# Optimization experiments

Measured on AMD Instinct MI355X. Metric: run time of the kernel, lower is better.

## Reference

```python
import jax, jax.numpy as jnp
import numpy as np

B, N, F_IN, D, DEPTH = 16, 1024, 80, 64, 4
BN_EPS = 1e-5

def setup_inputs() -> dict:
    key = jax.random.key(0)
    ks = jax.random.split(key, 24)
    def xavier(k, shape, gain):
        fan_in, fan_out = shape[0], shape[-1]
        a = gain * np.sqrt(6.0 / (fan_in + fan_out))
        return jax.random.uniform(k, shape, jnp.float32, -a, a)
    g_relu = float(np.sqrt(2.0))
    g_lrelu = float(np.sqrt(2.0 / (1 + 0.01 ** 2)))
    adj = jax.random.randint(ks[0], (B, N, N), 0, 2, jnp.int32)
    X = jax.random.normal(ks[1], (B, N, F_IN), jnp.float32)
    root_list = jax.random.randint(ks[2], (B, DEPTH, N), 0, 2).astype(jnp.float32)
    W0 = xavier(ks[3], (F_IN, D), g_lrelu)
    Wl = jnp.stack([xavier(ks[4 + i], (D, D), g_relu) for i in range(3)])
    a1l = jnp.stack([xavier(ks[7 + i], (D, 1), g_relu)[:, 0] for i in range(3)])
    a2l = jnp.stack([xavier(ks[10 + i], (D, 1), g_relu)[:, 0] for i in range(3)])
    P = xavier(ks[13], (1, D), g_relu)
    def linear(k, din, dout):
        a = 1.0 / np.sqrt(din)
        k1, k2 = jax.random.split(k)
        return (jax.random.uniform(k1, (din, dout), jnp.float32, -a, a),
                jax.random.uniform(k2, (dout,), jnp.float32, -a, a))
    pW1, pb1 = linear(ks[14], D, 128)
    pW2, pb2 = linear(ks[15], 128, 64)
    pW3, pb3 = linear(ks[16], 64, 2)
    bn = lambda n: (jnp.ones((n,), jnp.float32), jnp.zeros((n,), jnp.float32),
                    jnp.zeros((n,), jnp.float32), jnp.ones((n,), jnp.float32))
    g1, be1, m1, v1 = bn(128)
    g2, be2, m2, v2 = bn(64)
    return dict(adj=adj, X=X, root_list=root_list, W0=W0, Wl=Wl, a1l=a1l, a2l=a2l, P=P,
                pW1=pW1, pb1=pb1, g1=g1, be1=be1, m1=m1, v1=v1,
                pW2=pW2, pb2=pb2, g2=g2, be2=be2, m2=m2, v2=v2,
                pW3=pW3, pb3=pb3)

def reference(adj, X, root_list, W0, Wl, a1l, a2l, P,
              pW1, pb1, g1, be1, m1, v1, pW2, pb2, g2, be2, m2, v2, pW3, pb3):
    relu = jax.nn.relu
    # initial feature change
    h = relu(jnp.einsum('bnf,fd->bnd', X, W0))
    adj_pos = adj > 0
    for i in range(DEPTH - 1):
        root = root_list[:, DEPTH - 1 - i, :]            # [B,N]
        h0 = h
        hW = relu(jnp.einsum('bnd,de->bne', h, Wl[i]))    # [B,N,D]
        t1 = jnp.einsum('bnd,d->bn', hW, a1l[i])
        t2 = jnp.einsum('bnd,d->bn', hW, a2l[i])
        e = relu(t1[:, :, None] + t2[:, None, :])         # [B,N,N]
        # NOTE: original uses -9e15 * zeros_like(adj) == 0 as the masked fill value
        e = jnp.where(adj_pos, e, jnp.zeros((), e.dtype))
        att = jax.nn.softmax(e, axis=-1)
        emb = jnp.einsum('bnm,bmd->bnd', att, hW)
        # assign = root^T @ ones broadcasts root over d
        h = jnp.where(root[:, :, None] > 0, emb, h0)
    # readout attention over root nodes (last root used: depth index 1)
    root = root_list[:, 1, :]
    e = relu(jnp.einsum('d,bnd->bn', P[0], h))
    e = jnp.where(root > 0, e, jnp.float32(-9e15))
    att = jax.nn.softmax(e, axis=-1)
    out = jnp.einsum('bn,bnd->bd', att, h)                # [B,D]
    # prediction head (eval mode: BN uses running stats, dropout off)
    def bn_apply(x, g, be, m, v):
        return (x - m) * jax.lax.rsqrt(v + BN_EPS) * g + be
    x = relu(bn_apply(out @ pW1 + pb1, g1, be1, m1, v1))
    x = relu(bn_apply(x @ pW2 + pb2, g2, be2, m2, v2))
    logits = relu(x @ pW3 + pb3)
    return jax.nn.softmax(logits, axis=-1)
```

## Files before the change

### kernel.cpp

```cpp
#include <hip/hip_runtime.h>
#include <hip/hip_bf16.h>
#include <math.h>

#define B 16
#define N 1024
#define F_IN 80
#define D 64
#define DEPTH 4
#define BN_EPS 1e-5f

typedef __attribute__((ext_vector_type(8))) short  short8v;
typedef __attribute__((ext_vector_type(4))) float  float4v;

union AFrag { unsigned int u[4]; short8v s; };

__device__ __forceinline__ unsigned short f2bf_rne(float x) {
    unsigned int u = __float_as_uint(x);
    unsigned int r = u + 0x7FFFu + ((u >> 16) & 1u);
    return (unsigned short)(r >> 16);
}
__device__ __forceinline__ float bf2f(unsigned short b) {
    return __uint_as_float(((unsigned int)b) << 16);
}
__device__ __forceinline__ void split_pair(float w0, float w1,
                                           unsigned int& hi, unsigned int& lo) {
    unsigned int u0 = __float_as_uint(w0), u1 = __float_as_uint(w1);
    unsigned int h0 = u0 & 0xFFFF0000u,   h1 = u1 & 0xFFFF0000u;
    hi = (h0 >> 16) | h1;
    float r0 = w0 - __uint_as_float(h0);
    float r1 = w1 - __uint_as_float(h1);
    lo = (__float_as_uint(r0) >> 16) | (__float_as_uint(r1) & 0xFFFF0000u);
}

__global__ __launch_bounds__(256) void k_pre(const int* __restrict__ adj,
                                             unsigned short* __restrict__ packS,
                                             const float* __restrict__ X,
                                             const float* __restrict__ W0,
                                             float* __restrict__ h) {
    if (blockIdx.x < 4096) {
        int gid = blockIdx.x * 256 + threadIdx.x;
        const int4* ap = (const int4*)adj + (size_t)gid * 4;
        unsigned int m = 0;
#pragma unroll
        for (int i = 0; i < 4; ++i) {
            int4 v = ap[i];
            m |= (unsigned int)(v.x > 0) << (i * 4 + 0);
            m |= (unsigned int)(v.y > 0) << (i * 4 + 1);
            m |= (unsigned int)(v.z > 0) << (i * 4 + 2);
            m |= (unsigned int)(v.w > 0) << (i * 4 + 3);
        }
        packS[gid] = (unsigned short)m;
        return;
    }
    int bid = blockIdx.x - 4096;
    int b = bid >> 6, n0 = (bid & 63) << 4;
    int t = threadIdx.x;
    __shared__ float w0s[F_IN * D];
    __shared__ float xs[16 * F_IN];
    for (int j = t; j < F_IN * D / 4; j += 256)
        ((float4*)w0s)[j] = ((const float4*)W0)[j];
    const float* xp = X + ((size_t)(b * N + n0)) * F_IN;
    for (int j = t; j < 16 * F_IN / 4; j += 256)
        ((float4*)xs)[j] = ((const float4*)xp)[j];
    __syncthreads();
    int d = t & 63, wid = t >> 6;
    float acc[4] = {0.f, 0.f, 0.f, 0.f};
    for (int f = 0; f < F_IN; ++f) {
        float wv = w0s[f * D + d];
#pragma unroll
        for (int j = 0; j < 4; ++j) acc[j] += xs[(wid * 4 + j) * F_IN + f] * wv;
    }
    float* hp = h + ((size_t)(b * N + n0 + wid * 4)) * D + d;
#pragma unroll
    for (int j = 0; j < 4; ++j) hp[(size_t)j * D] = fmaxf(acc[j], 0.f);
}

__global__ __launch_bounds__(256) void k_hw(const float* __restrict__ h,
                                            const float* __restrict__ Wl,
                                            const float* __restrict__ a1,
                                            const float* __restrict__ a2,
                                            unsigned short* __restrict__ hWhi,
                                            unsigned short* __restrict__ hWlo,
                                            float* __restrict__ t1,
                                            float* __restrict__ t2) {
    int b = blockIdx.x >> 6, n0 = (blockIdx.x & 63) << 4;
    int t = threadIdx.x;
    __shared__ float wls[D * D];
    __shared__ float hs[16 * D];
    for (int j = t; j < D * D / 4; j += 256)
        ((float4*)wls)[j] = ((const float4*)Wl)[j];
    const float* hp = h + ((size_t)(b * N + n0)) * D;
    if (t < 16 * D / 4) ((float4*)hs)[t] = ((const float4*)hp)[t];
    __syncthreads();
    int d = t & 63, wid = t >> 6;
    float acc[4] = {0.f, 0.f, 0.f, 0.f};
    for (int k = 0; k < D; ++k) {
        float wv = wls[k * D + d];
#pragma unroll
        for (int j = 0; j < 4; ++j) acc[j] += hs[(wid * 4 + j) * D + k] * wv;
    }
    float a1d = a1[d], a2d = a2[d];

    float v[4];
    unsigned short vh[4], vl[4];
#pragma unroll
    for (int j = 0; j < 4; ++j) {
        v[j] = fmaxf(acc[j], 0.f);
        vh[j] = f2bf_rne(v[j]);
        vl[j] = f2bf_rne(v[j] - bf2f(vh[j]));
    }
    {
        int m0 = n0 + wid * 4;
        int kb = m0 >> 5, i0 = m0 & 7;
        int lb = ((m0 >> 3) & 3) * 16 + (d & 15), dt = d >> 4;
        size_t off = ((size_t)b * (N * D)) + ((kb * 4 + dt) * 64 + lb) * 8 + i0;
        uint2 hpack, lpack;
        hpack.x = (unsigned int)vh[0] | ((unsigned int)vh[1] << 16);
        hpack.y = (unsigned int)vh[2] | ((unsigned int)vh[3] << 16);
        lpack.x = (unsigned int)vl[0] | ((unsigned int)vl[1] << 16);
        lpack.y = (unsigned int)vl[2] | ((unsigned int)vl[3] << 16);
        *(uint2*)(hWhi + off) = hpack;
        *(uint2*)(hWlo + off) = lpack;
    }
#pragma unroll
    for (int j = 0; j < 4; ++j) {
        float p1 = v[j] * a1d, p2 = v[j] * a2d;
#pragma unroll
        for (int o = 32; o > 0; o >>= 1) {
            p1 += __shfl_down(p1, o);
            p2 += __shfl_down(p2, o);
        }
        if (d == 0) { t1[b * N + n0 + wid * 4 + j] = p1; t2[b * N + n0 + wid * 4 + j] = p2; }
    }
}

__global__ __launch_bounds__(256, 4) void k_att(
    const unsigned short* __restrict__ hWhi, const unsigned short* __restrict__ hWlo,
    const float* __restrict__ t1, const float* __restrict__ t2,
    const unsigned long long* __restrict__ packA,
    const float* __restrict__ root_list, int ridx, float* __restrict__ h)
{
    int vb = (blockIdx.x & 7) * 128 + (blockIdx.x >> 3);
    int b  = vb >> 6;
    int n0 = (vb & 63) << 4;
    int t = threadIdx.x, lane = t & 63, wid = t >> 6;

    __shared__ float t2s[N];
    __shared__ float redsum[4][16];
    __shared__ float invs[16];
    __shared__ float4v part[4][4][64];

    ((float4v*)t2s)[t] = ((const float4v*)(t2 + b * N))[t];
    __syncthreads();

    int r  = lane & 15;
    int qg = wid * 4 + (lane >> 4);
    int n  = n0 + r;
    float t1v = t1[b * N + n];
    const unsigned long long* prow = packA + ((size_t)(b * N + n)) * 16;
    const short8v* BH = (const short8v*)(hWhi + (size_t)b * (N * D));
    const short8v* BL = (const short8v*)(hWlo + (size_t)b * (N * D));

    float4v acc0 = {0,0,0,0}, acc1 = {0,0,0,0}, acc2 = {0,0,0,0}, acc3 = {0,0,0,0};
    float lsum = 0.f;

#pragma unroll 2
    for (int p = 0; p < 8; ++p) {
        int kb = p * 4 + wid;
        int bi = (kb * 4) * 64 + lane;
        short8v bh0 = BH[bi], bh1 = BH[bi + 64], bh2 = BH[bi + 128], bh3 = BH[bi + 192];
        short8v bl0 = BL[bi], bl1 = BL[bi + 64], bl2 = BL[bi + 128], bl3 = BL[bi + 192];

        unsigned long long word = prow[p * 2 + (qg >> 3)];
        unsigned int mbyte = (unsigned int)(word >> ((qg & 7) * 8)) & 0xFFu;

        const float* t2p = t2s + p * 128 + qg * 8;
        float4v ta = ((const float4v*)t2p)[0];
        float4v tb = ((const float4v*)t2p)[1];

        float wv[8];
#pragma unroll
        for (int i = 0; i < 8; ++i) {
            float t2v = (i < 4) ? ta[i & 3] : tb[i & 3];
            float e = ((mbyte >> i) & 1u) ? fmaxf(t1v + t2v, 0.f) : 0.f;
            float w = __expf(e);
            wv[i] = w;
            lsum += w;
        }

        AFrag fh, fl;
#pragma unroll
        for (int i = 0; i < 4; ++i)
            split_pair(wv[2 * i], wv[2 * i + 1], fh.u[i], fl.u[i]);

        acc0 = __builtin_amdgcn_mfma_f32_16x16x32_bf16(fh.s, bh0, acc0, 0, 0, 0);
        acc0 = __builtin_amdgcn_mfma_f32_16x16x32_bf16(fh.s, bl0, acc0, 0, 0, 0);
        acc0 = __builtin_amdgcn_mfma_f32_16x16x32_bf16(fl.s, bh0, acc0, 0, 0, 0);
        acc1 = __builtin_amdgcn_mfma_f32_16x16x32_bf16(fh.s, bh1, acc1, 0, 0, 0);
        acc1 = __builtin_amdgcn_mfma_f32_16x16x32_bf16(fh.s, bl1, acc1, 0, 0, 0);
        acc1 = __builtin_amdgcn_mfma_f32_16x16x32_bf16(fl.s, bh1, acc1, 0, 0, 0);
        acc2 = __builtin_amdgcn_mfma_f32_16x16x32_bf16(fh.s, bh2, acc2, 0, 0, 0);
        acc2 = __builtin_amdgcn_mfma_f32_16x16x32_bf16(fh.s, bl2, acc2, 0, 0, 0);
        acc2 = __builtin_amdgcn_mfma_f32_16x16x32_bf16(fl.s, bh2, acc2, 0, 0, 0);
        acc3 = __builtin_amdgcn_mfma_f32_16x16x32_bf16(fh.s, bh3, acc3, 0, 0, 0);
        acc3 = __builtin_amdgcn_mfma_f32_16x16x32_bf16(fh.s, bl3, acc3, 0, 0, 0);
        acc3 = __builtin_amdgcn_mfma_f32_16x16x32_bf16(fl.s, bh3, acc3, 0, 0, 0);
    }

    lsum += __shfl_xor(lsum, 16);
    lsum += __shfl_xor(lsum, 32);
    if (lane < 16) redsum[wid][lane] = lsum;

    part[wid][0][lane] = acc0;
    part[wid][1][lane] = acc1;
    part[wid][2][lane] = acc2;
    part[wid][3][lane] = acc3;
    __syncthreads();
    if (t < 16) invs[t] = 1.0f / (redsum[0][t] + redsum[1][t] + redsum[2][t] + redsum[3][t]);
    __syncthreads();

    int c = t & 63, rg = t >> 6;
    int ls = rg * 16 + (c & 15), dt = c >> 4;
    float4v s = part[0][dt][ls] + part[1][dt][ls] + part[2][dt][ls] + part[3][dt][ls];
    const float* rl = root_list + ((size_t)b * DEPTH + ridx) * N;
#pragma unroll
    for (int reg = 0; reg < 4; ++reg) {
        int rr = rg * 4 + reg;
        if (rl[n0 + rr] > 0.f)
            h[((size_t)(b * N + n0 + rr)) * D + c] = s[reg] * invs[rr];
    }
}

__global__ __launch_bounds__(256) void k_dotw(const float* __restrict__ h,
                                              const float* __restrict__ root_list,
                                              const float* __restrict__ P,
                                              float* __restrict__ wg) {
    int b = blockIdx.x >> 4, n0 = (blockIdx.x & 15) << 6;
    int t = threadIdx.x;
    int r = n0 + (t >> 2), sub = t & 3;
    const float4* hp = (const float4*)(h + ((size_t)(b * N + r)) * D + sub * 16);
    const float4* pp = (const float4*)(P + sub * 16);
    float s = 0.f;
#pragma unroll
    for (int i = 0; i < 4; ++i) {
        float4 hv = hp[i], pv = pp[i];
        s += hv.x * pv.x + hv.y * pv.y + hv.z * pv.z + hv.w * pv.w;
    }
    s += __shfl_xor(s, 1);
    s += __shfl_xor(s, 2);
    if (sub == 0) {
        float rv = root_list[((size_t)b * DEPTH + 1) * N + r];
        wg[b * N + r] = (rv > 0.f) ? fmaxf(s, 0.f) : -9e15f;
    }
}

__global__ __launch_bounds__(1024) void k_pool2(const float* __restrict__ h,
                       const float* __restrict__ wg,
                       const float* __restrict__ pW1, const float* __restrict__ pb1,
                       const float* __restrict__ g1, const float* __restrict__ be1,
                       const float* __restrict__ m1, const float* __restrict__ v1,
                       const float* __restrict__ pW2, const float* __restrict__ pb2,
                       const float* __restrict__ g2, const float* __restrict__ be2,
                       const float* __restrict__ m2, const float* __restrict__ v2,
                       const float* __restrict__ pW3, const float* __restrict__ pb3,
                       float* __restrict__ out) {
    int b = blockIdx.x, t = threadIdx.x, lane = t & 63, wid = t >> 6;
    __shared__ float ws[N];
    __shared__ float red[16];
    __shared__ float part[16][D];
    __shared__ float od[D];
    __shared__ float x1[128];
    __shared__ float x2[64];
    __shared__ float lg[2];

    const float* hb = h + (size_t)b * N * D;
    float sc = wg[b * N + t];

    float lmax = sc;
#pragma unroll
    for (int o = 32; o > 0; o >>= 1) lmax = fmaxf(lmax, __shfl_xor(lmax, o));
    if (lane == 0) red[wid] = lmax;
    __syncthreads();
    float bmax = red[0];
#pragma unroll
    for (int k = 1; k < 16; ++k) bmax = fmaxf(bmax, red[k]);
    __syncthreads();

    float e = __expf(sc - bmax);
    ws[t] = e;
    float lsumv = e;
#pragma unroll
    for (int o = 32; o > 0; o >>= 1) lsumv += __shfl_xor(lsumv, o);
    if (lane == 0) red[wid] = lsumv;
    __syncthreads();
    float bsum = 0.f;
#pragma unroll
    for (int k = 0; k < 16; ++k) bsum += red[k];
    float inv = 1.0f / bsum;

    float acc = 0.f;
    for (int n = wid * 64; n < wid * 64 + 64; ++n) acc += ws[n] * hb[(size_t)n * D + lane];
    part[wid][lane] = acc;
    __syncthreads();
    if (t < D) {
        float s = 0.f;
#pragma unroll
        for (int k = 0; k < 16; ++k) s += part[k][t];
        od[t] = s * inv;
    }
    __syncthreads();

    if (t < 128) {
        float s = pb1[t];
#pragma unroll
        for (int k = 0; k < D; ++k) s += od[k] * pW1[k * 128 + t];
        s = (s - m1[t]) * rsqrtf(v1[t] + BN_EPS) * g1[t] + be1[t];
        x1[t] = fmaxf(s, 0.f);
    }
    __syncthreads();
    if (t < 64) {
        float s = pb2[t];
#pragma unroll
        for (int k = 0; k < 128; ++k) s += x1[k] * pW2[k * 64 + t];
        s = (s - m2[t]) * rsqrtf(v2[t] + BN_EPS) * g2[t] + be2[t];
        x2[t] = fmaxf(s, 0.f);
    }
    __syncthreads();
    if (t < 2) {
        float s = pb3[t];
#pragma unroll
        for (int k = 0; k < 64; ++k) s += x2[k] * pW3[k * 2 + t];
        lg[t] = fmaxf(s, 0.f);
    }
    __syncthreads();
    if (t < 2) {
        float mm = fmaxf(lg[0], lg[1]);
        float e0 = __expf(lg[0] - mm), e1 = __expf(lg[1] - mm);
        out[b * 2 + t] = ((t == 0) ? e0 : e1) / (e0 + e1);
    }
}

extern "C" void kernel_launch(void* const* d_in, const int* in_sizes, int n_in,
                              void* d_out, int out_size, void* d_ws, size_t ws_size,
                              hipStream_t stream) {
    const int*   adj = (const int*)d_in[0];
    const float* X   = (const float*)d_in[1];
    const float* rl  = (const float*)d_in[2];
    const float* W0  = (const float*)d_in[3];
    const float* Wl  = (const float*)d_in[4];
    const float* a1l = (const float*)d_in[5];
    const float* a2l = (const float*)d_in[6];
    const float* P   = (const float*)d_in[7];
    const float* pW1 = (const float*)d_in[8];
    const float* pb1 = (const float*)d_in[9];
    const float* g1  = (const float*)d_in[10];
    const float* be1 = (const float*)d_in[11];
    const float* m1  = (const float*)d_in[12];
    const float* v1  = (const float*)d_in[13];
    const float* pW2 = (const float*)d_in[14];
    const float* pb2 = (const float*)d_in[15];
    const float* g2  = (const float*)d_in[16];
    const float* be2 = (const float*)d_in[17];
    const float* m2  = (const float*)d_in[18];
    const float* v2  = (const float*)d_in[19];
    const float* pW3 = (const float*)d_in[20];
    const float* pb3 = (const float*)d_in[21];
    float* out = (float*)d_out;

    float*          h    = (float*)d_ws;
    unsigned short* hWhi = (unsigned short*)(h + (size_t)B * N * D);
    unsigned short* hWlo = hWhi + (size_t)B * N * D;
    float*          t1   = (float*)(hWlo + (size_t)B * N * D);
    float*          t2   = t1 + B * N;
    unsigned long long* packA = (unsigned long long*)(t2 + B * N);
    float*          wg   = t1;

    k_pre<<<4096 + B * 64, 256, 0, stream>>>(adj, (unsigned short*)packA, X, W0, h);
    for (int i = 0; i < DEPTH - 1; ++i) {
        k_hw<<<B * 64, 256, 0, stream>>>(h, Wl + i * D * D, a1l + i * D, a2l + i * D,
                                         hWhi, hWlo, t1, t2);
        k_att<<<B * 64, 256, 0, stream>>>(hWhi, hWlo, t1, t2, packA, rl,
                                          DEPTH - 1 - i, h);
    }
    k_dotw<<<B * 16, 256, 0, stream>>>(h, rl, P, wg);
    k_pool2<<<B, 1024, 0, stream>>>(h, wg, pW1, pb1, g1, be1, m1, v1,
                                    pW2, pb2, g2, be2, m2, v2, pW3, pb3, out);
}
```

Measured before the change: 227.1 us.

## Process two 16-row query tiles per attention block to reuse hW fragments

Each k_att block now handles 32 query rows (two 16-row MFMA tiles) instead of 16, so every loaded hW hi/lo B-fragment feeds twice as many MFMAs. This halves the grid to B*32 blocks and halves global and L2 traffic for hW per output row. In exchange, register pressure roughly doubles (occupancy hint lowered to 2), shared memory for partials doubles, and the smaller grid gives the GPU fewer blocks to spread across its compute units.

```diff
diff --git a/kernel.cpp b/kernel.cpp
--- a/kernel.cpp
+++ b/kernel.cpp
@@ -134,35 +134,38 @@
     }
 }
 
-__global__ __launch_bounds__(256, 4) void k_att(
+__global__ __launch_bounds__(256, 2) void k_att(
     const unsigned short* __restrict__ hWhi, const unsigned short* __restrict__ hWlo,
     const float* __restrict__ t1, const float* __restrict__ t2,
     const unsigned long long* __restrict__ packA,
     const float* __restrict__ root_list, int ridx, float* __restrict__ h)
 {
-    int vb = (blockIdx.x & 7) * 128 + (blockIdx.x >> 3);
-    int b  = vb >> 6;
-    int n0 = (vb & 63) << 4;
+    int vb = (blockIdx.x & 7) * 64 + (blockIdx.x >> 3);
+    int b  = vb >> 5;
+    int n0 = (vb & 31) << 5;
     int t = threadIdx.x, lane = t & 63, wid = t >> 6;
 
     __shared__ float t2s[N];
-    __shared__ float redsum[4][16];
-    __shared__ float invs[16];
-    __shared__ float4v part[4][4][64];
+    __shared__ float redsum[2][4][16];
+    __shared__ float invs[32];
+    __shared__ float4v part[2][4][4][64];
 
     ((float4v*)t2s)[t] = ((const float4v*)(t2 + b * N))[t];
     __syncthreads();
 
     int r  = lane & 15;
     int qg = wid * 4 + (lane >> 4);
-    int n  = n0 + r;
-    float t1v = t1[b * N + n];
-    const unsigned long long* prow = packA + ((size_t)(b * N + n)) * 16;
+    int nA = n0 + r, nB = nA + 16;
+    float t1vA = t1[b * N + nA];
+    float t1vB = t1[b * N + nB];
+    const unsigned long long* prowA = packA + ((size_t)(b * N + nA)) * 16;
+    const unsigned long long* prowB = packA + ((size_t)(b * N + nB)) * 16;
     const short8v* BH = (const short8v*)(hWhi + (size_t)b * (N * D));
     const short8v* BL = (const short8v*)(hWlo + (size_t)b * (N * D));
 
-    float4v acc0 = {0,0,0,0}, acc1 = {0,0,0,0}, acc2 = {0,0,0,0}, acc3 = {0,0,0,0};
-    float lsum = 0.f;
+    float4v a0 = {0,0,0,0}, a1v = {0,0,0,0}, a2v = {0,0,0,0}, a3 = {0,0,0,0};
+    float4v b0 = {0,0,0,0}, b1v = {0,0,0,0}, b2v = {0,0,0,0}, b3 = {0,0,0,0};
+    float lsumA = 0.f, lsumB = 0.f;
 
 #pragma unroll 2
     for (int p = 0; p < 8; ++p) {
@@ -171,63 +174,95 @@
         short8v bh0 = BH[bi], bh1 = BH[bi + 64], bh2 = BH[bi + 128], bh3 = BH[bi + 192];
         short8v bl0 = BL[bi], bl1 = BL[bi + 64], bl2 = BL[bi + 128], bl3 = BL[bi + 192];
 
-        unsigned long long word = prow[p * 2 + (qg >> 3)];
-        unsigned int mbyte = (unsigned int)(word >> ((qg & 7) * 8)) & 0xFFu;
+        unsigned long long wordA = prowA[p * 2 + (qg >> 3)];
+        unsigned long long wordB = prowB[p * 2 + (qg >> 3)];
+        unsigned int mbA = (unsigned int)(wordA >> ((qg & 7) * 8)) & 0xFFu;
+        unsigned int mbB = (unsigned int)(wordB >> ((qg & 7) * 8)) & 0xFFu;
 
         const float* t2p = t2s + p * 128 + qg * 8;
         float4v ta = ((const float4v*)t2p)[0];
         float4v tb = ((const float4v*)t2p)[1];
 
-        float wv[8];
+        float wvA[8], wvB[8];
 #pragma unroll
         for (int i = 0; i < 8; ++i) {
             float t2v = (i < 4) ? ta[i & 3] : tb[i & 3];
-            float e = ((mbyte >> i) & 1u) ? fmaxf(t1v + t2v, 0.f) : 0.f;
-            float w = __expf(e);
-            wv[i] = w;
-            lsum += w;
+            float eA = ((mbA >> i) & 1u) ? fmaxf(t1vA + t2v, 0.f) : 0.f;
+            float eB = ((mbB >> i) & 1u) ? fmaxf(t1vB + t2v, 0.f) : 0.f;
+            float wA = __expf(eA), wB = __expf(eB);
+            wvA[i] = wA; lsumA += wA;
+            wvB[i] = wB; lsumB += wB;
         }
 
-        AFrag fh, fl;
-#pragma unroll
-        for (int i = 0; i < 4; ++i)
-            split_pair(wv[2 * i], wv[2 * i + 1], fh.u[i], fl.u[i]);
-
-        acc0 = __builtin_amdgcn_mfma_f32_16x16x32_bf16(fh.s, bh0, acc0, 0, 0, 0);
-        acc0 = __builtin_amdgcn_mfma_f32_16x16x32_bf16(fh.s, bl0, acc0, 0, 0, 0);
-        acc0 = __builtin_amdgcn_mfma_f32_16x16x32_bf16(fl.s, bh0, acc0, 0, 0, 0);
-        acc1 = __builtin_amdgcn_mfma_f32_16x16x32_bf16(fh.s, bh1, acc1, 0, 0, 0);
-        acc1 = __builtin_amdgcn_mfma_f32_16x16x32_bf16(fh.s, bl1, acc1, 0, 0, 0);
-        acc1 = __builtin_amdgcn_mfma_f32_16x16x32_bf16(fl.s, bh1, acc1, 0, 0, 0);
-        acc2 = __builtin_amdgcn_mfma_f32_16x16x32_bf16(fh.s, bh2, acc2, 0, 0, 0);
-        acc2 = __builtin_amdgcn_mfma_f32_16x16x32_bf16(fh.s, bl2, acc2, 0, 0, 0);
-        acc2 = __builtin_amdgcn_mfma_f32_16x16x32_bf16(fl.s, bh2, acc2, 0, 0, 0);
-        acc3 = __builtin_amdgcn_mfma_f32_16x16x32_bf16(fh.s, bh3, acc3, 0, 0, 0);
-        acc3 = __builtin_amdgcn_mfma_f32_16x16x32_bf16(fh.s, bl3, acc3, 0, 0, 0);
-        acc3 = __builtin_amdgcn_mfma_f32_16x16x32_bf16(fl.s, bh3, acc3, 0, 0, 0);
-    }
-
-    lsum += __shfl_xor(lsum, 16);
-    lsum += __shfl_xor(lsum, 32);
-    if (lane < 16) redsum[wid][lane] = lsum;
-
-    part[wid][0][lane] = acc0;
-    part[wid][1][lane] = acc1;
-    part[wid][2][lane] = acc2;
-    part[wid][3][lane] = acc3;
-    __syncthreads();
-    if (t < 16) invs[t] = 1.0f / (redsum[0][t] + redsum[1][t] + redsum[2][t] + redsum[3][t]);
+        AFrag fhA, flA, fhB, flB;
+#pragma unroll
+        for (int i = 0; i < 4; ++i) {
+            split_pair(wvA[2 * i], wvA[2 * i + 1], fhA.u[i], flA.u[i]);
+            split_pair(wvB[2 * i], wvB[2 * i + 1], fhB.u[i], flB.u[i]);
+        }
+
+        a0 = __builtin_amdgcn_mfma_f32_16x16x32_bf16(fhA.s, bh0, a0, 0, 0, 0);
+        a0 = __builtin_amdgcn_mfma_f32_16x16x32_bf16(fhA.s, bl0, a0, 0, 0, 0);
+        a0 = __builtin_amdgcn_mfma_f32_16x16x32_bf16(flA.s, bh0, a0, 0, 0, 0);
+        b0 = __builtin_amdgcn_mfma_f32_16x16x32_bf16(fhB.s, bh0, b0, 0, 0, 0);
+        b0 = __builtin_amdgcn_mfma_f32_16x16x32_bf16(fhB.s, bl0, b0, 0, 0, 0);
+        b0 = __builtin_amdgcn_mfma_f32_16x16x32_bf16(flB.s, bh0, b0, 0, 0, 0);
+        a1v = __builtin_amdgcn_mfma_f32_16x16x32_bf16(fhA.s, bh1, a1v, 0, 0, 0);
+        a1v = __builtin_amdgcn_mfma_f32_16x16x32_bf16(fhA.s, bl1, a1v, 0, 0, 0);
+        a1v = __builtin_amdgcn_mfma_f32_16x16x32_bf16(flA.s, bh1, a1v, 0, 0, 0);
+        b1v = __builtin_amdgcn_mfma_f32_16x16x32_bf16(fhB.s, bh1, b1v, 0, 0, 0);
+        b1v = __builtin_amdgcn_mfma_f32_16x16x32_bf16(fhB.s, bl1, b1v, 0, 0, 0);
+        b1v = __builtin_amdgcn_mfma_f32_16x16x32_bf16(flB.s, bh1, b1v, 0, 0, 0);
+        a2v = __builtin_amdgcn_mfma_f32_16x16x32_bf16(fhA.s, bh2, a2v, 0, 0, 0);
+        a2v = __builtin_amdgcn_mfma_f32_16x16x32_bf16(fhA.s, bl2, a2v, 0, 0, 0);
+        a2v = __builtin_amdgcn_mfma_f32_16x16x32_bf16(flA.s, bh2, a2v, 0, 0, 0);
+        b2v = __builtin_amdgcn_mfma_f32_16x16x32_bf16(fhB.s, bh2, b2v, 0, 0, 0);
+        b2v = __builtin_amdgcn_mfma_f32_16x16x32_bf16(fhB.s, bl2, b2v, 0, 0, 0);
+        b2v = __builtin_amdgcn_mfma_f32_16x16x32_bf16(flB.s, bh2, b2v, 0, 0, 0);
+        a3 = __builtin_amdgcn_mfma_f32_16x16x32_bf16(fhA.s, bh3, a3, 0, 0, 0);
+        a3 = __builtin_amdgcn_mfma_f32_16x16x32_bf16(fhA.s, bl3, a3, 0, 0, 0);
+        a3 = __builtin_amdgcn_mfma_f32_16x16x32_bf16(flA.s, bh3, a3, 0, 0, 0);
+        b3 = __builtin_amdgcn_mfma_f32_16x16x32_bf16(fhB.s, bh3, b3, 0, 0, 0);
+        b3 = __builtin_amdgcn_mfma_f32_16x16x32_bf16(fhB.s, bl3, b3, 0, 0, 0);
+        b3 = __builtin_amdgcn_mfma_f32_16x16x32_bf16(flB.s, bh3, b3, 0, 0, 0);
+    }
+
+    lsumA += __shfl_xor(lsumA, 16);
+    lsumA += __shfl_xor(lsumA, 32);
+    lsumB += __shfl_xor(lsumB, 16);
+    lsumB += __shfl_xor(lsumB, 32);
+    if (lane < 16) { redsum[0][wid][lane] = lsumA; redsum[1][wid][lane] = lsumB; }
+
+    part[0][wid][0][lane] = a0;
+    part[0][wid][1][lane] = a1v;
+    part[0][wid][2][lane] = a2v;
+    part[0][wid][3][lane] = a3;
+    part[1][wid][0][lane] = b0;
+    part[1][wid][1][lane] = b1v;
+    part[1][wid][2][lane] = b2v;
+    part[1][wid][3][lane] = b3;
+    __syncthreads();
+    if (t < 32) {
+        int s = t >> 4, rr = t & 15;
+        invs[s * 16 + rr] = 1.0f / (redsum[s][0][rr] + redsum[s][1][rr] +
+                                    redsum[s][2][rr] + redsum[s][3][rr]);
+    }
     __syncthreads();
 
     int c = t & 63, rg = t >> 6;
     int ls = rg * 16 + (c & 15), dt = c >> 4;
-    float4v s = part[0][dt][ls] + part[1][dt][ls] + part[2][dt][ls] + part[3][dt][ls];
     const float* rl = root_list + ((size_t)b * DEPTH + ridx) * N;
 #pragma unroll
-    for (int reg = 0; reg < 4; ++reg) {
-        int rr = rg * 4 + reg;
-        if (rl[n0 + rr] > 0.f)
-            h[((size_t)(b * N + n0 + rr)) * D + c] = s[reg] * invs[rr];
+    for (int s = 0; s < 2; ++s) {
+        float4v sv = part[s][0][dt][ls] + part[s][1][dt][ls] +
+                     part[s][2][dt][ls] + part[s][3][dt][ls];
+#pragma unroll
+        for (int reg = 0; reg < 4; ++reg) {
+            int rr = rg * 4 + reg;
+            int n = n0 + s * 16 + rr;
+            if (rl[n] > 0.f)
+                h[((size_t)(b * N + n)) * D + c] = sv[reg] * invs[s * 16 + rr];
+        }
     }
 }
 
@@ -379,7 +414,7 @@
     for (int i = 0; i < DEPTH - 1; ++i) {
         k_hw<<<B * 64, 256, 0, stream>>>(h, Wl + i * D * D, a1l + i * D, a2l + i * D,
                                          hWhi, hWlo, t1, t2);
-        k_att<<<B * 64, 256, 0, stream>>>(hWhi, hWlo, t1, t2, packA, rl,
+        k_att<<<B * 32, 256, 0, stream>>>(hWhi, hWlo, t1, t2, packA, rl,
                                           DEPTH - 1 - i, h);
     }
     k_dotw<<<B * 16, 256, 0, stream>>>(h, rl, P, wg);
```

New measurement: 220.8 us. 1.03x faster.
